# Kernel tuning notes

Measured on AMD Instinct MI355X. Metric: run time of the kernel, lower is better.

Reference implementation:

```python
import jax, jax.numpy as jnp
import numpy as np

NUM_HEADS = 16


def rotate_half(x):
    h = x.shape[-1] // 2
    return jnp.concatenate([-x[..., h:], x[..., :h]], axis=-1)


def setup_inputs() -> dict:
    key = jax.random.key(0)
    ks = jax.random.split(key, 8)
    S, dim, hd = 8192, 1280, 80
    n_seg = 8
    hidden_states = jax.random.normal(ks[0], (S, dim), dtype=jnp.float32)
    cu_seqlens = (jnp.arange(n_seg + 1, dtype=jnp.int32) * (S // n_seg))
    ang = jax.random.uniform(ks[1], (S, hd), dtype=jnp.float32) * (2.0 * np.pi)
    cos = jnp.cos(ang)
    sin = jnp.sin(ang)
    qkv_w = jax.random.normal(ks[2], (3 * dim, dim), dtype=jnp.float32) * (dim ** -0.5)
    qkv_b = jax.random.normal(ks[3], (3 * dim,), dtype=jnp.float32) * 0.02
    proj_w = jax.random.normal(ks[4], (dim, dim), dtype=jnp.float32) * (dim ** -0.5)
    proj_b = jax.random.normal(ks[5], (dim,), dtype=jnp.float32) * 0.02
    return {"hidden_states": hidden_states, "cu_seqlens": cu_seqlens,
            "cos": cos, "sin": sin, "qkv_w": qkv_w, "qkv_b": qkv_b,
            "proj_w": proj_w, "proj_b": proj_b}


def reference(hidden_states, cu_seqlens, cos, sin, qkv_w, qkv_b, proj_w, proj_b):
    S, dim = hidden_states.shape
    H = NUM_HEADS
    hd = dim // H
    scaling = hd ** -0.5

    # qkv projection: [S, 3*dim] -> [S, 3, H, hd]
    qkv = (hidden_states @ qkv_w.T + qkv_b).reshape(S, 3, H, hd)
    q, k, v = qkv[:, 0], qkv[:, 1], qkv[:, 2]  # each [S, H, hd]

    # RoPE in float32, cos/sin broadcast over heads
    c = cos[:, None, :].astype(jnp.float32)
    s = sin[:, None, :].astype(jnp.float32)
    qf, kf = q.astype(jnp.float32), k.astype(jnp.float32)
    q = (qf * c + rotate_half(qf) * s).astype(q.dtype)
    k = (kf * c + rotate_half(kf) * s).astype(k.dtype)

    # Block-diagonal varlen attention: equal-length segments -> batch dim
    lengths = np.diff(np.asarray(cu_seqlens))
    L = int(lengths[0])
    assert (lengths == L).all(), "reference assumes uniform segment lengths"
    B = lengths.shape[0]
    qb = q.reshape(B, L, H, hd)
    kb = k.reshape(B, L, H, hd)
    vb = v.reshape(B, L, H, hd)

    scores = jnp.einsum('blhd,bmhd->bhlm', qb, kb) * scaling
    probs = jax.nn.softmax(scores.astype(jnp.float32), axis=-1).astype(scores.dtype)
    out = jnp.einsum('bhlm,bmhd->blhd', probs, vb).reshape(S, dim)

    return out @ proj_w.T + proj_b
```

## Files before the change

kernel.cpp:

```cpp
#include <hip/hip_runtime.h>
#include <math.h>

typedef _Float16 f16;
typedef _Float16 half8 __attribute__((ext_vector_type(8)));
typedef _Float16 half4v __attribute__((ext_vector_type(4)));
typedef _Float16 half2v __attribute__((ext_vector_type(2)));
typedef float floatx4 __attribute__((ext_vector_type(4)));
typedef unsigned int u32;

#define AS1 __attribute__((address_space(1)))
#define AS3 __attribute__((address_space(3)))

__device__ __forceinline__ void stage16(f16* l, const f16* g) {
    __builtin_amdgcn_global_load_lds((const AS1 u32*)g, (AS3 u32*)l, 16, 0, 0);
}

__global__ __launch_bounds__(256) void cvt_f32_f16(const float* __restrict__ in,
                                                   f16* __restrict__ out, int n4) {
    int i = blockIdx.x * blockDim.x + threadIdx.x;
    if (i >= n4) return;
    float4 v = ((const float4*)in)[i];
    half4v h = {(f16)v.x, (f16)v.y, (f16)v.z, (f16)v.w};
    ((half4v*)out)[i] = h;
}

__global__ __launch_bounds__(256) void pack_w(const float* __restrict__ Wf,
                                              f16* __restrict__ Wp) {
    const int p = blockIdx.x * 256 + threadIdx.x;
    const int lane = p & 63;
    const int j = (p >> 6) & 3;
    const int sk = p >> 8;
    const int k0 = sk % 40;
    const int slab = sk / 40;
    const int row = slab * 64 + j * 16 + (lane & 15);
    const int col = k0 * 32 + (lane >> 4) * 8;
    const float* src = Wf + (size_t)row * 1280 + col;
    float4 a = *(const float4*)src;
    float4 b = *(const float4*)(src + 4);
    half8 h = {(f16)a.x, (f16)a.y, (f16)a.z, (f16)a.w,
               (f16)b.x, (f16)b.y, (f16)b.z, (f16)b.w};
    *(half8*)(Wp + (size_t)p * 8) = h;
}

constexpr int GK = 1280;
constexpr int KT = 20;

template <int MT>
__global__ __launch_bounds__(512, 2) void gemm_bp(const f16* __restrict__ A,
                                                  const f16* __restrict__ Bp,
                                                  const float* __restrict__ bias,
                                                  f16* __restrict__ outH,
                                                  float* __restrict__ outF,
                                                  int N, int NT) {
    constexpr int M_FR = MT / 32;
    constexpr int QE = MT * 32;
    __shared__ f16 sm[2][2][QE];
    const int t = threadIdx.x;
    const int lane = t & 63, w = t >> 6;
    const int wm = w >> 2, wn = w & 3;
    const int c16 = lane & 15, quad = lane >> 4;
    const int id = blockIdx.x;
    const int nx = (int)gridDim.x >> 3;
    const int gid = (id & 7) * nx + (id >> 3);
    const int bm = gid / NT, bn = gid - bm * NT;
    const f16* Ab = A + (size_t)bm * MT * GK;
    const f16* Bw = Bp + (size_t)(bn * 4 + wn) * (40 * 4 * 64 * 8) + lane * 8;

    floatx4 acc[M_FR][4] = {};
    half8 bfA[8], bfB[8];

    auto stageA = [&](int kt, int dst) {
#pragma unroll
        for (int ks = 0; ks < 2; ks++)
#pragma unroll
            for (int u = 0; u < MT / 128; u++) {
                const int c = t + u * 512;
                const int row = c >> 2;
                const int lc = ((c & 3) - (row >> 1)) & 3;
                stage16(&sm[dst][ks][0] + c * 8,
                        Ab + (size_t)row * GK + kt * 64 + ks * 32 + lc * 8);
            }
    };
    auto loadB = [&](int kt, half8(&bf)[8]) {
#pragma unroll
        for (int ks = 0; ks < 2; ks++)
#pragma unroll
            for (int j = 0; j < 4; j++)
                bf[ks * 4 + j] = *(const half8*)(Bw + (size_t)((kt * 2 + ks) * 4 + j) * 512);
    };
    auto compute = [&](int p, half8(&bf)[8]) {
#pragma unroll
        for (int ks = 0; ks < 2; ks++) {
            const f16* q = &sm[p][ks][0];
#pragma unroll
            for (int m = 0; m < M_FR; m++) {
                const int r = wm * (MT / 2) + m * 16 + c16;
                half8 a = *(const half8*)(q + r * 32 + (((quad + (r >> 1)) & 3) * 8));
#pragma unroll
                for (int n = 0; n < 4; n++)
                    acc[m][n] = __builtin_amdgcn_mfma_f32_16x16x32_f16(a, bf[ks * 4 + n],
                                                                       acc[m][n], 0, 0, 0);
            }
        }
    };
#define WAIT_STEADY()                                              \
    if constexpr (MT == 256) {                                     \
        asm volatile("s_waitcnt vmcnt(12)" ::: "memory");          \
    } else {                                                       \
        asm volatile("s_waitcnt vmcnt(10)" ::: "memory");          \
    }

    stageA(0, 0);
    loadB(0, bfA);
    asm volatile("s_waitcnt vmcnt(8)" ::: "memory");
    __builtin_amdgcn_s_barrier();

    for (int i = 0; i < 10; i++) {
        const int k0 = 2 * i;
        asm volatile("s_waitcnt lgkmcnt(0)" ::: "memory");
        __builtin_amdgcn_s_barrier();
        stageA(k0 + 1, 1);
        loadB(k0 + 1, bfB);
        WAIT_STEADY();
        __builtin_amdgcn_s_barrier();
        compute(0, bfA);
        asm volatile("s_waitcnt lgkmcnt(0)" ::: "memory");
        __builtin_amdgcn_s_barrier();
        if (i < 9) {
            stageA(k0 + 2, 0);
            loadB(k0 + 2, bfA);
            WAIT_STEADY();
        } else {
            asm volatile("s_waitcnt vmcnt(0)" ::: "memory");
        }
        __builtin_amdgcn_s_barrier();
        compute(1, bfB);
    }

    const int colBase = bn * 256 + wn * 64;
    const size_t rowBase = (size_t)bm * MT + wm * (MT / 2);
    float bv[4];
#pragma unroll
    for (int n = 0; n < 4; n++) bv[n] = bias[colBase + n * 16 + c16];
#pragma unroll
    for (int m = 0; m < M_FR; m++) {
#pragma unroll
        for (int r = 0; r < 4; r++) {
            const size_t row = rowBase + m * 16 + quad * 4 + r;
#pragma unroll
            for (int n = 0; n < 4; n++) {
                const int col = colBase + n * 16 + c16;
                const float v = acc[m][n][r] + bv[n];
                if (outH) outH[row * (size_t)N + col] = (f16)v;
                else      outF[row * (size_t)N + col] = v;
            }
        }
    }
}

#define QSCALE (0.11180339887498949f * 1.4426950408889634f)

__global__ __launch_bounds__(320) void rope_kernel(const f16* __restrict__ qkv,
                                                   const float* __restrict__ cosp,
                                                   const float* __restrict__ sinp,
                                                   f16* __restrict__ qb, f16* __restrict__ kb,
                                                   f16* __restrict__ vt) {
    constexpr int S = 8192;
    const int bs = blockIdx.x, h = blockIdx.y, t = threadIdx.x;
    const int sl = t / 5, g = t % 5;
    const int s = bs * 64 + sl;
    {
        const size_t base = (size_t)s * 3840 + h * 80 + g * 8;
        half8 qa = *(const half8*)(qkv + base);
        half8 qc = *(const half8*)(qkv + base + 40);
        half8 ka = *(const half8*)(qkv + base + 1280);
        half8 kc = *(const half8*)(qkv + base + 1320);
        const float* cp = cosp + (size_t)s * 80 + g * 8;
        const float* sp = sinp + (size_t)s * 80 + g * 8;
        half8 qo0, qo1, ko0, ko1;
#pragma unroll
        for (int j = 0; j < 8; j++) {
            float c0 = cp[j], c1 = cp[j + 40];
            float n0 = sp[j], n1 = sp[j + 40];
            float q0 = (float)qa[j], q1 = (float)qc[j];
            float k0 = (float)ka[j], k1 = (float)kc[j];
            qo0[j] = (f16)((q0 * c0 - q1 * n0) * QSCALE);
            qo1[j] = (f16)((q1 * c1 + q0 * n1) * QSCALE);
            ko0[j] = (f16)(k0 * c0 - k1 * n0);
            ko1[j] = (f16)(k1 * c1 + k0 * n1);
        }
        const size_t ob = ((size_t)h * S + s) * 96 + g * 8;
        *(half8*)(qb + ob)      = qo0;
        *(half8*)(qb + ob + 40) = qo1;
        *(half8*)(kb + ob)      = ko0;
        *(half8*)(kb + ob + 40) = ko1;
        if (g < 2) {
            half8 qp = {}, kp = {};
            if (g == 0) { qp[0] = (f16)(-8.0f); kp[0] = (f16)(1.0f); }
            const size_t pb = ((size_t)h * S + s) * 96 + 80 + g * 8;
            *(half8*)(qb + pb) = qp;
            *(half8*)(kb + pb) = kp;
        }
    }
    __shared__ f16 vls[64][81];
    for (int j = t; j < 64 * 80; j += 320) {
        int s2 = j / 80, d = j % 80;
        vls[s2][d] = qkv[((size_t)(bs * 64 + s2)) * 3840 + 2560 + h * 80 + d];
    }
    __syncthreads();
    for (int j = t; j < 64 * 80; j += 320) {
        int d = j >> 6, s2 = j & 63;
        vt[((size_t)(h * 80 + d)) * S + bs * 64 + s2] = vls[s2][d];
    }
}

__global__ __launch_bounds__(256, 2) void attn_kernel(const f16* __restrict__ qb,
                                                      const f16* __restrict__ kb,
                                                      const f16* __restrict__ vt,
                                                      const int* __restrict__ cu,
                                                      f16* __restrict__ out) {
    constexpr int S = 8192;
    __shared__ f16 Ks[2][64 * 96];
    __shared__ f16 Ps[256 * 72];
    const int t = threadIdx.x, lane = t & 63, w = t >> 6;
    const int c16 = lane & 15, quad = lane >> 4;
    const int id = blockIdx.x;
    const int pair = id & 127;
    const int qt = id >> 7;
    const int h = pair & 15, z = pair >> 4;
    const int s0 = cu[z];

    half8 qf[4][3];
#pragma unroll
    for (int qt2 = 0; qt2 < 4; qt2++)
#pragma unroll
        for (int ks = 0; ks < 3; ks++)
            qf[qt2][ks] = *(const half8*)(qb + ((size_t)h * S + s0 + qt * 256 + w * 64 + qt2 * 16 + c16) * 96 + ks * 32 + quad * 8);

    const f16 ov = (c16 == 0) ? (f16)1.f : (f16)0.f;
    const half8 onesf = {ov, ov, ov, ov, ov, ov, ov, ov};

    const int sR = t >> 2;
    const int sK = ((t & 3) - (sR >> 1)) & 3;

    {
        const f16* Kg = kb + ((size_t)h * S + s0) * 96;
#pragma unroll
        for (int j = 0; j < 3; j++)
            stage16(&Ks[0][0] + (j * 256 + t) * 8, Kg + (size_t)sR * 96 + j * 32 + sK * 8);
    }
    __syncthreads();

    floatx4 o[6][4] = {};

    for (int kv = 0; kv < 16; kv++) {
        if (kv < 15) {
            const f16* Kg = kb + ((size_t)h * S + s0 + (kv + 1) * 64) * 96;
            f16* Kd = &Ks[(kv + 1) & 1][0];
#pragma unroll
            for (int j = 0; j < 3; j++)
                stage16(Kd + (j * 256 + t) * 8, Kg + (size_t)sR * 96 + j * 32 + sK * 8);
        }
        const f16* Kc = &Ks[kv & 1][0];
        floatx4 sc[4][4] = {};
#pragma unroll
        for (int ks = 0; ks < 3; ks++) {
            half8 kf[4];
#pragma unroll
            for (int mt = 0; mt < 4; mt++) {
                const int row = mt * 16 + c16;
                kf[mt] = *(const half8*)(Kc + (ks * 256 + 4 * row + ((quad + (row >> 1)) & 3)) * 8);
            }
#pragma unroll
            for (int qt2 = 0; qt2 < 4; qt2++)
#pragma unroll
                for (int mt = 0; mt < 4; mt++)
                    sc[mt][qt2] = __builtin_amdgcn_mfma_f32_16x16x32_f16(kf[mt], qf[qt2][ks], sc[mt][qt2], 0, 0, 0);
        }
#pragma unroll
        for (int qt2 = 0; qt2 < 4; qt2++) {
            const int q = w * 64 + qt2 * 16 + c16;
#pragma unroll
            for (int mt = 0; mt < 4; mt++) {
                half4v pv;
#pragma unroll
                for (int r = 0; r < 4; r++)
                    pv[r] = (f16)__builtin_amdgcn_exp2f(sc[mt][qt2][r]);
                *(half4v*)(Ps + q * 72 + mt * 16 + quad * 4) = pv;
            }
        }
#pragma unroll
        for (int ks = 0; ks < 2; ks++) {
            const f16* Vg = vt + (size_t)h * 80 * S + s0 + kv * 64 + ks * 32;
            half8 vf[5];
#pragma unroll
            for (int dt = 0; dt < 5; dt++)
                vf[dt] = *(const half8*)(Vg + (size_t)(dt * 16 + c16) * S + quad * 8);
#pragma unroll
            for (int qt2 = 0; qt2 < 4; qt2++) {
                const int q = w * 64 + qt2 * 16 + c16;
                half8 pf = *(const half8*)(Ps + q * 72 + ks * 32 + quad * 8);
#pragma unroll
                for (int dt = 0; dt < 5; dt++)
                    o[dt][qt2] = __builtin_amdgcn_mfma_f32_16x16x32_f16(vf[dt], pf, o[dt][qt2], 0, 0, 0);
                o[5][qt2] = __builtin_amdgcn_mfma_f32_16x16x32_f16(onesf, pf, o[5][qt2], 0, 0, 0);
            }
        }
        __syncthreads();
    }
#pragma unroll
    for (int qt2 = 0; qt2 < 4; qt2++) {
        const float l = __shfl(o[5][qt2][0], c16);
        const float inv = 1.f / l;
        const size_t srow = (size_t)s0 + qt * 256 + w * 64 + qt2 * 16 + c16;
#pragma unroll
        for (int dt = 0; dt < 5; dt++)
#pragma unroll
            for (int rp = 0; rp < 2; rp++) {
                half2v hv = {(f16)(o[dt][qt2][rp * 2] * inv), (f16)(o[dt][qt2][rp * 2 + 1] * inv)};
                *(half2v*)(out + srow * 1280 + h * 80 + dt * 16 + quad * 4 + rp * 2) = hv;
            }
    }
}

extern "C" void kernel_launch(void* const* d_in, const int* in_sizes, int n_in,
                              void* d_out, int out_size, void* d_ws, size_t ws_size,
                              hipStream_t stream) {
    const float* hidden = (const float*)d_in[0];
    const int* cu       = (const int*)d_in[1];
    const float* cosp   = (const float*)d_in[2];
    const float* sinp   = (const float*)d_in[3];
    const float* qkv_w  = (const float*)d_in[4];
    const float* qkv_b  = (const float*)d_in[5];
    const float* proj_w = (const float*)d_in[6];
    const float* proj_b = (const float*)d_in[7];
    float* out = (float*)d_out;

    constexpr size_t S = 8192, DIM = 1280, N3 = 3840;
    f16* A16   = (f16*)d_ws;
    f16* WP16  = A16 + S * DIM;
    f16* PP16  = WP16 + N3 * DIM;
    f16* QKV16 = PP16 + DIM * DIM;
    f16* QB    = QKV16 + S * N3;
    f16* KB    = QB + (size_t)16 * S * 96;
    f16* VT    = KB + (size_t)16 * S * 96;
    f16* AT16  = A16;

    {
        int n4 = (int)(S * DIM / 4);
        cvt_f32_f16<<<(n4 + 255) / 256, 256, 0, stream>>>(hidden, A16, n4);
    }
    pack_w<<<(int)(N3 * DIM / 8 / 256), 256, 0, stream>>>(qkv_w, WP16);
    pack_w<<<(int)(DIM * DIM / 8 / 256), 256, 0, stream>>>(proj_w, PP16);
    gemm_bp<256><<<32 * 15, 512, 0, stream>>>(A16, WP16, qkv_b, QKV16, nullptr, 3840, 15);
    rope_kernel<<<dim3(128, 16), 320, 0, stream>>>(QKV16, cosp, sinp, QB, KB, VT);
    attn_kernel<<<512, 256, 0, stream>>>(QB, KB, VT, cu, A16);
    gemm_bp<128><<<64 * 5, 512, 0, stream>>>(AT16, PP16, proj_b, nullptr, out, 1280, 5);
}
```

Measured before the change: 375.8 us.

## Triple-buffer A tiles in GEMM LDS pipeline and raise MFMA wave priority

The GEMM's shared-memory staging of A goes from two buffers to three, so A tiles are prefetched two k-steps ahead instead of one, and the vmcnt waits are retuned to match. The compute phase is also wrapped in s_setprio(1)/s_setprio(0) so MFMA-issuing waves get scheduling priority. The goal is to hide more global-load latency behind the matrix math. In exchange LDS use rises by half (significant for MT=256 at two blocks per CU), which may cut occupancy, and the hand-counted vmcnt values must exactly match the number of loads in flight.

New measurement: 381.1 us. About the same (+1.4%).

```diff
diff --git a/kernel.cpp b/kernel.cpp
--- a/kernel.cpp
+++ b/kernel.cpp
@@ -54,7 +54,7 @@
                                                   int N, int NT) {
     constexpr int M_FR = MT / 32;
     constexpr int QE = MT * 32;
-    __shared__ f16 sm[2][2][QE];
+    __shared__ f16 sm[3][2][QE];
     const int t = threadIdx.x;
     const int lane = t & 63, w = t >> 6;
     const int wm = w >> 2, wn = w & 3;
@@ -88,10 +88,11 @@
             for (int j = 0; j < 4; j++)
                 bf[ks * 4 + j] = *(const half8*)(Bw + (size_t)((kt * 2 + ks) * 4 + j) * 512);
     };
-    auto compute = [&](int p, half8(&bf)[8]) {
+    auto compute = [&](int b, half8(&bf)[8]) {
+        __builtin_amdgcn_s_setprio(1);
 #pragma unroll
         for (int ks = 0; ks < 2; ks++) {
-            const f16* q = &sm[p][ks][0];
+            const f16* q = &sm[b][ks][0];
 #pragma unroll
             for (int m = 0; m < M_FR; m++) {
                 const int r = wm * (MT / 2) + m * 16 + c16;
@@ -102,39 +103,34 @@
                                                                        acc[m][n], 0, 0, 0);
             }
         }
+        __builtin_amdgcn_s_setprio(0);
     };
-#define WAIT_STEADY()                                              \
-    if constexpr (MT == 256) {                                     \
-        asm volatile("s_waitcnt vmcnt(12)" ::: "memory");          \
-    } else {                                                       \
-        asm volatile("s_waitcnt vmcnt(10)" ::: "memory");          \
-    }
 
     stageA(0, 0);
     loadB(0, bfA);
-    asm volatile("s_waitcnt vmcnt(8)" ::: "memory");
-    __builtin_amdgcn_s_barrier();
+    stageA(1, 1);
 
     for (int i = 0; i < 10; i++) {
-        const int k0 = 2 * i;
+        const int kt = 2 * i;
         asm volatile("s_waitcnt lgkmcnt(0)" ::: "memory");
         __builtin_amdgcn_s_barrier();
-        stageA(k0 + 1, 1);
-        loadB(k0 + 1, bfB);
-        WAIT_STEADY();
+        loadB(kt + 1, bfB);
+        if (i < 9) stageA(kt + 2, (kt + 2) % 3);
+        if (i < 9) { asm volatile("s_waitcnt vmcnt(16)" ::: "memory"); }
+        else       { asm volatile("s_waitcnt vmcnt(12)" ::: "memory"); }
         __builtin_amdgcn_s_barrier();
-        compute(0, bfA);
+        compute(kt % 3, bfA);
         asm volatile("s_waitcnt lgkmcnt(0)" ::: "memory");
         __builtin_amdgcn_s_barrier();
         if (i < 9) {
-            stageA(k0 + 2, 0);
-            loadB(k0 + 2, bfA);
-            WAIT_STEADY();
+            loadB(kt + 2, bfA);
+            stageA(kt + 3, (kt + 3) % 3);
+            asm volatile("s_waitcnt vmcnt(16)" ::: "memory");
         } else {
             asm volatile("s_waitcnt vmcnt(0)" ::: "memory");
         }
         __builtin_amdgcn_s_barrier();
-        compute(1, bfB);
+        compute((kt + 1) % 3, bfB);
     }
 
     const int colBase = bn * 256 + wn * 64;
```

## Read K directly from global in attention, add setprio, new proj GEMM kernel

Applied to the files above, without the earlier changes.

The attention kernel drops its double-buffered LDS staging of K tiles and per-iteration block barrier, and instead has each wave load K fragments straight from global memory. It also raises wave priority around the MFMA bursts. The output projection moves from gemm_bp<128> to a new 128x128-tile 256-thread GEMM, gemm_nt, which stages A through LDS and reads packed B from global. Removing the barrier and LDS traffic trades for redundant global/L2 reads of K across the four waves. Dropping the __syncthreads may also risk a race on the shared Ps buffer, although each wave appears to use only its own rows.

After: 373.1 us. Within noise of the previous version (-0.7%).

```diff
diff --git a/kernel.cpp b/kernel.cpp
--- a/kernel.cpp
+++ b/kernel.cpp
@@ -158,6 +158,63 @@
     }
 }
 
+__global__ __launch_bounds__(256) void gemm_nt(const f16* __restrict__ A,
+                                               const f16* __restrict__ Bp,
+                                               const float* __restrict__ bias,
+                                               f16* __restrict__ outH,
+                                               float* __restrict__ outF, int N) {
+    __shared__ f16 As[128 * 32];
+    const int t = threadIdx.x;
+    const int lane = t & 63;
+    const int w = t >> 6;
+    const int wm = w & 1, wn = w >> 1;
+    const int c16 = lane & 15, quad = lane >> 4;
+    const size_t bm = blockIdx.x, bn = blockIdx.y;
+    const f16* Ab = A + bm * 128 * GK;
+    const f16* Bw = Bp + (size_t)(bn * 2 + wn) * (40 * 4 * 64 * 8);
+    floatx4 acc[4][4] = {};
+    const int c0 = t, c1 = t + 256;
+    const int r0 = c0 >> 2, kc0 = ((c0 & 3) - (r0 >> 1)) & 3;
+    const int r1 = c1 >> 2, kc1 = ((c1 & 3) - (r1 >> 1)) & 3;
+    for (int k0i = 0; k0i < 40; k0i++) {
+        const int k0 = k0i * 32;
+        stage16(As + c0 * 8, Ab + (size_t)r0 * GK + k0 + kc0 * 8);
+        stage16(As + c1 * 8, Ab + (size_t)r1 * GK + k0 + kc1 * 8);
+        half8 bf[4];
+#pragma unroll
+        for (int j = 0; j < 4; j++)
+            bf[j] = *(const half8*)(Bw + (((size_t)k0i * 4 + j) * 64 + lane) * 8);
+        __syncthreads();
+        half8 af[4];
+#pragma unroll
+        for (int i = 0; i < 4; i++) {
+            const int row = wm * 64 + i * 16 + c16;
+            af[i] = *(const half8*)(As + (4 * row + ((quad + (row >> 1)) & 3)) * 8);
+        }
+#pragma unroll
+        for (int i = 0; i < 4; i++)
+#pragma unroll
+            for (int j = 0; j < 4; j++)
+                acc[i][j] = __builtin_amdgcn_mfma_f32_16x16x32_f16(af[i], bf[j], acc[i][j], 0, 0, 0);
+        __syncthreads();
+    }
+#pragma unroll
+    for (int i = 0; i < 4; i++) {
+#pragma unroll
+        for (int j = 0; j < 4; j++) {
+            const int col = (int)bn * 128 + wn * 64 + j * 16 + c16;
+            const float bv = bias[col];
+#pragma unroll
+            for (int r = 0; r < 4; r++) {
+                const size_t row = bm * 128 + wm * 64 + i * 16 + quad * 4 + r;
+                const float v = acc[i][j][r] + bv;
+                if (outH) outH[row * (size_t)N + col] = (f16)v;
+                else      outF[row * (size_t)N + col] = v;
+            }
+        }
+    }
+}
+
 #define QSCALE (0.11180339887498949f * 1.4426950408889634f)
 
 __global__ __launch_bounds__(320) void rope_kernel(const f16* __restrict__ qkv,
@@ -220,7 +277,6 @@
                                                       const int* __restrict__ cu,
                                                       f16* __restrict__ out) {
     constexpr int S = 8192;
-    __shared__ f16 Ks[2][64 * 96];
     __shared__ f16 Ps[256 * 72];
     const int t = threadIdx.x, lane = t & 63, w = t >> 6;
     const int c16 = lane & 15, quad = lane >> 4;
@@ -240,42 +296,24 @@
     const f16 ov = (c16 == 0) ? (f16)1.f : (f16)0.f;
     const half8 onesf = {ov, ov, ov, ov, ov, ov, ov, ov};
 
-    const int sR = t >> 2;
-    const int sK = ((t & 3) - (sR >> 1)) & 3;
-
-    {
-        const f16* Kg = kb + ((size_t)h * S + s0) * 96;
-#pragma unroll
-        for (int j = 0; j < 3; j++)
-            stage16(&Ks[0][0] + (j * 256 + t) * 8, Kg + (size_t)sR * 96 + j * 32 + sK * 8);
-    }
-    __syncthreads();
-
     floatx4 o[6][4] = {};
 
     for (int kv = 0; kv < 16; kv++) {
-        if (kv < 15) {
-            const f16* Kg = kb + ((size_t)h * S + s0 + (kv + 1) * 64) * 96;
-            f16* Kd = &Ks[(kv + 1) & 1][0];
-#pragma unroll
-            for (int j = 0; j < 3; j++)
-                stage16(Kd + (j * 256 + t) * 8, Kg + (size_t)sR * 96 + j * 32 + sK * 8);
-        }
-        const f16* Kc = &Ks[kv & 1][0];
+        const f16* Kg = kb + ((size_t)h * S + s0 + kv * 64) * 96;
         floatx4 sc[4][4] = {};
 #pragma unroll
         for (int ks = 0; ks < 3; ks++) {
             half8 kf[4];
 #pragma unroll
-            for (int mt = 0; mt < 4; mt++) {
-                const int row = mt * 16 + c16;
-                kf[mt] = *(const half8*)(Kc + (ks * 256 + 4 * row + ((quad + (row >> 1)) & 3)) * 8);
-            }
+            for (int mt = 0; mt < 4; mt++)
+                kf[mt] = *(const half8*)(Kg + (size_t)(mt * 16 + c16) * 96 + ks * 32 + quad * 8);
+            __builtin_amdgcn_s_setprio(1);
 #pragma unroll
             for (int qt2 = 0; qt2 < 4; qt2++)
 #pragma unroll
                 for (int mt = 0; mt < 4; mt++)
                     sc[mt][qt2] = __builtin_amdgcn_mfma_f32_16x16x32_f16(kf[mt], qf[qt2][ks], sc[mt][qt2], 0, 0, 0);
+            __builtin_amdgcn_s_setprio(0);
         }
 #pragma unroll
         for (int qt2 = 0; qt2 < 4; qt2++) {
@@ -300,13 +338,14 @@
             for (int qt2 = 0; qt2 < 4; qt2++) {
                 const int q = w * 64 + qt2 * 16 + c16;
                 half8 pf = *(const half8*)(Ps + q * 72 + ks * 32 + quad * 8);
+                __builtin_amdgcn_s_setprio(1);
 #pragma unroll
                 for (int dt = 0; dt < 5; dt++)
                     o[dt][qt2] = __builtin_amdgcn_mfma_f32_16x16x32_f16(vf[dt], pf, o[dt][qt2], 0, 0, 0);
                 o[5][qt2] = __builtin_amdgcn_mfma_f32_16x16x32_f16(onesf, pf, o[5][qt2], 0, 0, 0);
-            }
-        }
-        __syncthreads();
+                __builtin_amdgcn_s_setprio(0);
+            }
+        }
     }
 #pragma unroll
     for (int qt2 = 0; qt2 < 4; qt2++) {
@@ -355,5 +394,5 @@
     gemm_bp<256><<<32 * 15, 512, 0, stream>>>(A16, WP16, qkv_b, QKV16, nullptr, 3840, 15);
     rope_kernel<<<dim3(128, 16), 320, 0, stream>>>(QKV16, cosp, sinp, QB, KB, VT);
     attn_kernel<<<512, 256, 0, stream>>>(QB, KB, VT, cu, A16);
-    gemm_bp<128><<<64 * 5, 512, 0, stream>>>(AT16, PP16, proj_b, nullptr, out, 1280, 5);
-}
+    gemm_nt<<<dim3(64, 10), 256, 0, stream>>>(AT16, PP16, proj_b, nullptr, out, 1280);
+}
```
